# Kernel optimization log

Measured on AMD Instinct MI355X. Metric: run time of the kernel, lower is better.

## Reference

```python
import jax, jax.numpy as jnp
import numpy as np

SEQ, B, IN, H, L = 2048, 64, 512, 512, 2

def _xavier(key, shape):
    fan_out, fan_in = shape
    bound = float(np.sqrt(6.0 / (fan_in + fan_out)))
    return jax.random.uniform(key, shape, jnp.float32, -bound, bound)

def setup_inputs() -> dict:
    key = jax.random.key(0)
    ks = jax.random.split(key, 5)
    x = jax.random.normal(ks[0], (SEQ, B, IN), jnp.float32)
    # layer 0: input_size=IN; layer 1: input_size=H. Biases init to zeros (reset_parameters).
    return {
        "x": x,
        "W_ih0": _xavier(ks[1], (H, IN)),
        "W_hh0": _xavier(ks[2], (H, H)),
        "b_ih0": jnp.zeros((H,), jnp.float32),
        "b_hh0": jnp.zeros((H,), jnp.float32),
        "W_ih1": _xavier(ks[3], (H, H)),
        "W_hh1": _xavier(ks[4], (H, H)),
        "b_ih1": jnp.zeros((H,), jnp.float32),
        "b_hh1": jnp.zeros((H,), jnp.float32),
    }

def _run_layer(x_in, W_ih, W_hh, b_ih, b_hh):
    # Precompute input projection for all timesteps (matches forward_optimized / same math as forward).
    proj = jnp.einsum('sbi,hi->sbh', x_in, W_ih) + b_ih  # [S,B,H]
    h0 = jnp.zeros((x_in.shape[1], W_hh.shape[0]), x_in.dtype)
    def step(h, p_t):
        h_new = jnp.tanh(p_t + h @ W_hh.T + b_hh)
        return h_new, h_new
    h_final, outs = jax.lax.scan(step, h0, proj)
    return outs, h_final

def reference(x, W_ih0, W_hh0, b_ih0, b_hh0, W_ih1, W_hh1, b_ih1, b_hh1):
    out0, h0 = _run_layer(x, W_ih0, W_hh0, b_ih0, b_hh0)
    out1, h1 = _run_layer(out0, W_ih1, W_hh1, b_ih1, b_hh1)
    hidden = jnp.stack([h0, h1], axis=0)  # [num_layers, B, H]
    return out1, hidden
```

## Files before the change

kernel.cpp:

```cpp
#include <hip/hip_runtime.h>
#include <cstdint>
#include <cstddef>

#define SEQ   2048
#define BATCH 64
#define HID   512

__global__ __launch_bounds__(256)
void proj_gemm(const float* __restrict__ A, const float* __restrict__ W,
               const float* __restrict__ bias, float* __restrict__ C)
{
    __shared__ float As[16][132];
    __shared__ float Bs[16][132];
    const int t  = threadIdx.x;
    const int bm = blockIdx.x >> 2;
    const int bn = blockIdx.x & 3;
    const int m0 = bm * 128;
    const int n0 = bn * 128;
    const int tn = t & 15;
    const int tm = t >> 4;

    float acc[8][8];
#pragma unroll
    for (int i = 0; i < 8; ++i)
#pragma unroll
        for (int j = 0; j < 8; ++j) acc[i][j] = 0.f;

    const int lrow = t >> 2;
    const int lk4  = t & 3;

    for (int kk = 0; kk < 512; kk += 16) {
#pragma unroll
        for (int i = 0; i < 2; ++i) {
            const int row = lrow + i * 64;
            float4 va = *(const float4*)&A[(size_t)(m0 + row) * 512 + kk + lk4 * 4];
            As[lk4 * 4 + 0][row] = va.x;
            As[lk4 * 4 + 1][row] = va.y;
            As[lk4 * 4 + 2][row] = va.z;
            As[lk4 * 4 + 3][row] = va.w;
            float4 vb = *(const float4*)&W[(size_t)(n0 + row) * 512 + kk + lk4 * 4];
            Bs[lk4 * 4 + 0][row] = vb.x;
            Bs[lk4 * 4 + 1][row] = vb.y;
            Bs[lk4 * 4 + 2][row] = vb.z;
            Bs[lk4 * 4 + 3][row] = vb.w;
        }
        __syncthreads();
#pragma unroll
        for (int k = 0; k < 16; ++k) {
            float4 a0 = *(const float4*)&As[k][tm * 8];
            float4 a1 = *(const float4*)&As[k][tm * 8 + 4];
            float4 b0 = *(const float4*)&Bs[k][tn * 4];
            float4 b1 = *(const float4*)&Bs[k][64 + tn * 4];
            float ar[8] = {a0.x, a0.y, a0.z, a0.w, a1.x, a1.y, a1.z, a1.w};
            float bc[8] = {b0.x, b0.y, b0.z, b0.w, b1.x, b1.y, b1.z, b1.w};
#pragma unroll
            for (int i = 0; i < 8; ++i)
#pragma unroll
                for (int j = 0; j < 8; ++j)
                    acc[i][j] = fmaf(ar[i], bc[j], acc[i][j]);
        }
        __syncthreads();
    }

    float4 bv0 = *(const float4*)&bias[n0 + tn * 4];
    float4 bv1 = *(const float4*)&bias[n0 + 64 + tn * 4];
    const float bb[8] = {bv0.x, bv0.y, bv0.z, bv0.w, bv1.x, bv1.y, bv1.z, bv1.w};
#pragma unroll
    for (int i = 0; i < 8; ++i) {
        const size_t rowoff = (size_t)(m0 + tm * 8 + i) * 512 + n0;
        float4 o0, o1;
        o0.x = acc[i][0] + bb[0]; o0.y = acc[i][1] + bb[1];
        o0.z = acc[i][2] + bb[2]; o0.w = acc[i][3] + bb[3];
        o1.x = acc[i][4] + bb[4]; o1.y = acc[i][5] + bb[5];
        o1.z = acc[i][6] + bb[6]; o1.w = acc[i][7] + bb[7];
        *(float4*)&C[rowoff + tn * 4] = o0;
        *(float4*)&C[rowoff + 64 + tn * 4] = o1;
    }
}

__device__ __forceinline__ float fast_tanh(float x)
{
    const float e = __builtin_amdgcn_exp2f(x * 2.88539008177793f);
    return fmaf(-2.0f, __builtin_amdgcn_rcpf(e + 1.0f), 1.0f);
}

#define WLD(i)  const float4 w##i = wb[(i) * 64]
#define WFMA(i, accA, accB) do { \
    const float4 hp = h0[i]; const float4 hq = h1[i]; \
    accA = fmaf(w##i.x, hp.x, accA); accA = fmaf(w##i.y, hp.y, accA); \
    accA = fmaf(w##i.z, hp.z, accA); accA = fmaf(w##i.w, hp.w, accA); \
    accB = fmaf(w##i.x, hq.x, accB); accB = fmaf(w##i.y, hq.y, accB); \
    accB = fmaf(w##i.z, hq.z, accB); accB = fmaf(w##i.w, hq.w, accB); } while (0)

__global__ __launch_bounds__(512, 2)
void rnn_scan(const float* __restrict__ proj, const float* __restrict__ Whh,
              const float* __restrict__ bhh, float* __restrict__ out,
              float* __restrict__ hidden, unsigned long long* __restrict__ hbuf)
{
    extern __shared__ float lds[];
    float4* Wv4 = (float4*)lds;
    float4* hS4 = (float4*)(lds + 32768);
    float*  hSf = lds + 32768;

    const int t    = threadIdx.x;
    const int bid  = blockIdx.x;
    const int g    = bid & 31;
    const int s    = bid >> 5;
    const int b0   = g * 2;
    const int base = s * 64;
    const int w    = t >> 6;
    const int l    = t & 63;
    const int rr   = l & 7;
    const int kc   = l >> 3;
    const int row  = base + w * 8 + rr;

    const float4* Wg4 = (const float4*)Whh;
    {
        const int k0 = kc * 16;
#pragma unroll
        for (int j = 0; j < 16; ++j)
            Wv4[w * 1024 + j * 64 + l] = Wg4[(size_t)row * 128 + k0 + j];
    }
    const bool pub  = (kc < 2);
    const float breg = pub ? bhh[row] : 0.f;

    for (int i = t; i < 2176; i += 512) hSf[i] = 0.f;
    __syncthreads();

    const bool own  = (t >= base) && (t < base + 64);
    const int  pado = (t >> 6) * 68 + (t & 63);

    float pv_next = 0.f;
    if (pub) pv_next = proj[(size_t)(b0 + kc) * HID + row];

    unsigned long long* gb = hbuf + (size_t)g * 4096;
    const float4* wb = Wv4 + w * 1024 + l;

    for (int step = 0; step < SEQ; ++step) {
        const int p = step & 1;

        const float pv = pv_next;
        if (pub && step + 1 < SEQ)
            pv_next = proj[((size_t)(step + 1) * BATCH + (b0 + kc)) * HID + row];

        WLD(0);  WLD(1);  WLD(2);  WLD(3);
        WLD(4);  WLD(5);  WLD(6);  WLD(7);
        WLD(8);  WLD(9);  WLD(10); WLD(11);
        WLD(12); WLD(13); WLD(14); WLD(15);
        __builtin_amdgcn_sched_barrier(0);

        if (!own) {
            const unsigned int want = (unsigned int)step;
            const unsigned long long* f0 = gb + (size_t)p * 2048 + t;
            const unsigned long long* f1 = f0 + 512;
            unsigned long long x0 = 0, x1 = 0;
            bool ok0 = false, ok1 = false;
            int spins = 0;
            for (;;) {
                if (!ok0) {
                    x0 = __hip_atomic_load(f0, __ATOMIC_RELAXED, __HIP_MEMORY_SCOPE_AGENT);
                    ok0 = (unsigned int)(x0 >> 32) == want;
                }
                if (!ok1) {
                    x1 = __hip_atomic_load(f1, __ATOMIC_RELAXED, __HIP_MEMORY_SCOPE_AGENT);
                    ok1 = (unsigned int)(x1 >> 32) == want;
                }
                if (ok0 & ok1) break;
                __builtin_amdgcn_s_sleep(1);
                if (++spins > 4096) {
                    __builtin_amdgcn_fence(__ATOMIC_ACQUIRE, "agent");
                    spins = 0;
                }
            }
            hSf[p * 1088 + pado]       = __uint_as_float((unsigned int)x0);
            hSf[p * 1088 + 544 + pado] = __uint_as_float((unsigned int)x1);
        }
        __syncthreads();

        const float4* h0 = hS4 + p * 272 + kc * 17;
        const float4* h1 = h0 + 136;
        float a0e = 0.f, a0o = 0.f, a1e = 0.f, a1o = 0.f;
        WFMA(0,  a0e, a1e); WFMA(1,  a0o, a1o);
        WFMA(2,  a0e, a1e); WFMA(3,  a0o, a1o);
        WFMA(4,  a0e, a1e); WFMA(5,  a0o, a1o);
        WFMA(6,  a0e, a1e); WFMA(7,  a0o, a1o);
        WFMA(8,  a0e, a1e); WFMA(9,  a0o, a1o);
        WFMA(10, a0e, a1e); WFMA(11, a0o, a1o);
        WFMA(12, a0e, a1e); WFMA(13, a0o, a1o);
        WFMA(14, a0e, a1e); WFMA(15, a0o, a1o);
        float s0 = a0e + a0o;
        float s1 = a1e + a1o;
        s0 += __shfl_xor(s0, 8, 64);  s1 += __shfl_xor(s1, 8, 64);
        s0 += __shfl_xor(s0, 16, 64); s1 += __shfl_xor(s1, 16, 64);
        s0 += __shfl_xor(s0, 32, 64); s1 += __shfl_xor(s1, 32, 64);

        if (pub) {
            const float sum = (kc == 0) ? s0 : s1;
            const int   bb  = b0 + kc;
            const float hn  = fast_tanh(pv + breg + sum);
            out[((size_t)step * BATCH + bb) * HID + row] = hn;
            const unsigned long long pk =
                ((unsigned long long)(unsigned int)(step + 1) << 32) |
                (unsigned long long)__float_as_uint(hn);
            __hip_atomic_store(gb + (size_t)(p ^ 1) * 2048 + (size_t)kc * 512 + row,
                               pk, __ATOMIC_RELAXED, __HIP_MEMORY_SCOPE_AGENT);
            hSf[(p ^ 1) * 1088 + kc * 544 + (row >> 6) * 68 + (row & 63)] = hn;
            if (step == SEQ - 1) hidden[(size_t)bb * HID + row] = hn;
        }
    }
}

extern "C" void kernel_launch(void* const* d_in, const int* in_sizes, int n_in,
                              void* d_out, int out_size, void* d_ws, size_t ws_size,
                              hipStream_t stream)
{
    (void)in_sizes; (void)n_in; (void)out_size; (void)ws_size;

    const float* x    = (const float*)d_in[0];
    const float* Wih0 = (const float*)d_in[1];
    const float* Whh0 = (const float*)d_in[2];
    const float* bih0 = (const float*)d_in[3];
    const float* bhh0 = (const float*)d_in[4];
    const float* Wih1 = (const float*)d_in[5];
    const float* Whh1 = (const float*)d_in[6];
    const float* bih1 = (const float*)d_in[7];
    const float* bhh1 = (const float*)d_in[8];

    float* out1   = (float*)d_out;
    float* hidden = out1 + (size_t)SEQ * BATCH * HID;

    float* proj = (float*)d_ws;
    unsigned long long* hbufA = (unsigned long long*)(proj + (size_t)SEQ * BATCH * HID);
    unsigned long long* hbufB = hbufA + (size_t)32 * 4096;

    hipMemsetAsync(hbufA, 0, (size_t)2 * 32 * 4096 * sizeof(unsigned long long),
                   stream);

    const size_t shmem = (size_t)(32768 + 2176) * sizeof(float);
    (void)hipFuncSetAttribute((const void*)rnn_scan,
                              hipFuncAttributeMaxDynamicSharedMemorySize, (int)shmem);

    proj_gemm<<<dim3(4096), dim3(256), 0, stream>>>(x, Wih0, bih0, proj);
    {
        const float* p = proj; const float* w = Whh0; const float* bb = bhh0;
        float* o = out1; float* hd = hidden; unsigned long long* hb = hbufA;
        void* args[] = {&p, &w, &bb, &o, &hd, &hb};
        hipLaunchCooperativeKernel((const void*)rnn_scan, dim3(256), dim3(512),
                                   args, (unsigned)shmem, stream);
    }

    proj_gemm<<<dim3(4096), dim3(256), 0, stream>>>(out1, Wih1, bih1, proj);
    {
        const float* p = proj; const float* w = Whh1; const float* bb = bhh1;
        float* o = out1; float* hd = hidden + BATCH * HID; unsigned long long* hb = hbufB;
        void* args[] = {&p, &w, &bb, &o, &hd, &hb};
        hipLaunchCooperativeKernel((const void*)rnn_scan, dim3(256), dim3(512),
                                   args, (unsigned)shmem, stream);
    }
}
```

Measured before the change: 9.570 ms.

## Stream bf16-converted recurrent weights from global memory instead of LDS

W_hh is pre-converted into a permuted bf16 layout by a new conversion kernel. Each scan step now reads those weights straight from global memory with inline-asm dwordx2 loads, instead of staging the fp32 weights in 128KB of LDS. The goal is to halve the weight bytes per step and free LDS, issuing the loads early so they overlap the cross-block spin-wait. In exchange, weight reads now go to L2 on the sequential critical path every step. bf16 rounding of the recurrent weights accumulates error over 2048 steps. The inline-asm loads also rely on implicit waitcnts being inserted before their results are used.

Result: slower. 13.55 ms (+41.6%).

```diff
diff --git a/kernel.cpp b/kernel.cpp
--- a/kernel.cpp
+++ b/kernel.cpp
@@ -78,29 +78,51 @@
     }
 }
 
+__device__ __forceinline__ unsigned short f2bf(float f)
+{
+    const unsigned int u = __float_as_uint(f);
+    return (unsigned short)((u + 0x7fffu + ((u >> 16) & 1u)) >> 16);
+}
+
+__global__ __launch_bounds__(256)
+void conv_bf16(const float* __restrict__ W, ushort4* __restrict__ dst)
+{
+    const int i   = blockIdx.x * 256 + threadIdx.x;
+    const int row = i & 511;
+    const int kj  = i >> 9;
+    const int k0  = ((kj >> 4) << 6) | ((kj & 15) << 2);
+    const float4 v = *(const float4*)&W[(size_t)row * 512 + k0];
+    ushort4 o;
+    o.x = f2bf(v.x); o.y = f2bf(v.y); o.z = f2bf(v.z); o.w = f2bf(v.w);
+    dst[i] = o;
+}
+
 __device__ __forceinline__ float fast_tanh(float x)
 {
     const float e = __builtin_amdgcn_exp2f(x * 2.88539008177793f);
     return fmaf(-2.0f, __builtin_amdgcn_rcpf(e + 1.0f), 1.0f);
 }
 
-#define WLD(i)  const float4 w##i = wb[(i) * 64]
+#define WISSUE(i) asm volatile("global_load_dwordx2 %0, %1, off" \
+                               : "=v"(wv##i) : "v"(wb + (i) * 512))
 #define WFMA(i, accA, accB) do { \
-    const float4 hp = h0[i]; const float4 hq = h1[i]; \
-    accA = fmaf(w##i.x, hp.x, accA); accA = fmaf(w##i.y, hp.y, accA); \
-    accA = fmaf(w##i.z, hp.z, accA); accA = fmaf(w##i.w, hp.w, accA); \
-    accB = fmaf(w##i.x, hq.x, accB); accB = fmaf(w##i.y, hq.y, accB); \
-    accB = fmaf(w##i.z, hq.z, accB); accB = fmaf(w##i.w, hq.w, accB); } while (0)
+    const float4 ha = h0[i]; const float4 hb = h1[i]; \
+    const float f0 = __uint_as_float(wv##i.x << 16); \
+    const float f1 = __uint_as_float(wv##i.x & 0xffff0000u); \
+    const float f2 = __uint_as_float(wv##i.y << 16); \
+    const float f3 = __uint_as_float(wv##i.y & 0xffff0000u); \
+    accA = fmaf(f0, ha.x, accA); accA = fmaf(f1, ha.y, accA); \
+    accA = fmaf(f2, ha.z, accA); accA = fmaf(f3, ha.w, accA); \
+    accB = fmaf(f0, hb.x, accB); accB = fmaf(f1, hb.y, accB); \
+    accB = fmaf(f2, hb.z, accB); accB = fmaf(f3, hb.w, accB); } while (0)
 
 __global__ __launch_bounds__(512, 2)
-void rnn_scan(const float* __restrict__ proj, const float* __restrict__ Whh,
+void rnn_scan(const float* __restrict__ proj, const ushort4* __restrict__ Wbf,
               const float* __restrict__ bhh, float* __restrict__ out,
               float* __restrict__ hidden, unsigned long long* __restrict__ hbuf)
 {
-    extern __shared__ float lds[];
-    float4* Wv4 = (float4*)lds;
-    float4* hS4 = (float4*)(lds + 32768);
-    float*  hSf = lds + 32768;
+    __shared__ float hSf[2176];
+    float4* hS4 = (float4*)hSf;
 
     const int t    = threadIdx.x;
     const int bid  = blockIdx.x;
@@ -111,17 +133,10 @@
     const int w    = t >> 6;
     const int l    = t & 63;
     const int rr   = l & 7;
-    const int kc   = l >> 3;
+    const int kq   = l >> 3;
     const int row  = base + w * 8 + rr;
 
-    const float4* Wg4 = (const float4*)Whh;
-    {
-        const int k0 = kc * 16;
-#pragma unroll
-        for (int j = 0; j < 16; ++j)
-            Wv4[w * 1024 + j * 64 + l] = Wg4[(size_t)row * 128 + k0 + j];
-    }
-    const bool pub  = (kc < 2);
+    const bool pub  = (kq < 2);
     const float breg = pub ? bhh[row] : 0.f;
 
     for (int i = t; i < 2176; i += 512) hSf[i] = 0.f;
@@ -131,23 +146,24 @@
     const int  pado = (t >> 6) * 68 + (t & 63);
 
     float pv_next = 0.f;
-    if (pub) pv_next = proj[(size_t)(b0 + kc) * HID + row];
+    if (pub) pv_next = proj[(size_t)(b0 + kq) * HID + row];
 
     unsigned long long* gb = hbuf + (size_t)g * 4096;
-    const float4* wb = Wv4 + w * 1024 + l;
+    const ushort4* wb = Wbf + (size_t)(kq << 4) * 512 + row;
 
     for (int step = 0; step < SEQ; ++step) {
         const int p = step & 1;
 
         const float pv = pv_next;
         if (pub && step + 1 < SEQ)
-            pv_next = proj[((size_t)(step + 1) * BATCH + (b0 + kc)) * HID + row];
-
-        WLD(0);  WLD(1);  WLD(2);  WLD(3);
-        WLD(4);  WLD(5);  WLD(6);  WLD(7);
-        WLD(8);  WLD(9);  WLD(10); WLD(11);
-        WLD(12); WLD(13); WLD(14); WLD(15);
-        __builtin_amdgcn_sched_barrier(0);
+            pv_next = proj[((size_t)(step + 1) * BATCH + (b0 + kq)) * HID + row];
+
+        uint2 wv0, wv1, wv2, wv3, wv4, wv5, wv6, wv7;
+        uint2 wv8, wv9, wv10, wv11, wv12, wv13, wv14, wv15;
+        WISSUE(0);  WISSUE(1);  WISSUE(2);  WISSUE(3);
+        WISSUE(4);  WISSUE(5);  WISSUE(6);  WISSUE(7);
+        WISSUE(8);  WISSUE(9);  WISSUE(10); WISSUE(11);
+        WISSUE(12); WISSUE(13); WISSUE(14); WISSUE(15);
 
         if (!own) {
             const unsigned int want = (unsigned int)step;
@@ -177,7 +193,7 @@
         }
         __syncthreads();
 
-        const float4* h0 = hS4 + p * 272 + kc * 17;
+        const float4* h0 = hS4 + p * 272 + kq * 17;
         const float4* h1 = h0 + 136;
         float a0e = 0.f, a0o = 0.f, a1e = 0.f, a1o = 0.f;
         WFMA(0,  a0e, a1e); WFMA(1,  a0o, a1o);
@@ -195,16 +211,16 @@
         s0 += __shfl_xor(s0, 32, 64); s1 += __shfl_xor(s1, 32, 64);
 
         if (pub) {
-            const float sum = (kc == 0) ? s0 : s1;
-            const int   bb  = b0 + kc;
+            const float sum = (kq == 0) ? s0 : s1;
+            const int   bb  = b0 + kq;
             const float hn  = fast_tanh(pv + breg + sum);
             out[((size_t)step * BATCH + bb) * HID + row] = hn;
             const unsigned long long pk =
                 ((unsigned long long)(unsigned int)(step + 1) << 32) |
                 (unsigned long long)__float_as_uint(hn);
-            __hip_atomic_store(gb + (size_t)(p ^ 1) * 2048 + (size_t)kc * 512 + row,
+            __hip_atomic_store(gb + (size_t)(p ^ 1) * 2048 + (size_t)kq * 512 + row,
                                pk, __ATOMIC_RELAXED, __HIP_MEMORY_SCOPE_AGENT);
-            hSf[(p ^ 1) * 1088 + kc * 544 + (row >> 6) * 68 + (row & 63)] = hn;
+            hSf[(p ^ 1) * 1088 + kq * 544 + (row >> 6) * 68 + (row & 63)] = hn;
             if (step == SEQ - 1) hidden[(size_t)bb * HID + row] = hn;
         }
     }
@@ -232,29 +248,30 @@
     float* proj = (float*)d_ws;
     unsigned long long* hbufA = (unsigned long long*)(proj + (size_t)SEQ * BATCH * HID);
     unsigned long long* hbufB = hbufA + (size_t)32 * 4096;
+    ushort4* Wbf0 = (ushort4*)(hbufB + (size_t)32 * 4096);
+    ushort4* Wbf1 = Wbf0 + 65536;
 
     hipMemsetAsync(hbufA, 0, (size_t)2 * 32 * 4096 * sizeof(unsigned long long),
                    stream);
 
-    const size_t shmem = (size_t)(32768 + 2176) * sizeof(float);
-    (void)hipFuncSetAttribute((const void*)rnn_scan,
-                              hipFuncAttributeMaxDynamicSharedMemorySize, (int)shmem);
+    conv_bf16<<<dim3(256), dim3(256), 0, stream>>>(Whh0, Wbf0);
+    conv_bf16<<<dim3(256), dim3(256), 0, stream>>>(Whh1, Wbf1);
 
     proj_gemm<<<dim3(4096), dim3(256), 0, stream>>>(x, Wih0, bih0, proj);
     {
-        const float* p = proj; const float* w = Whh0; const float* bb = bhh0;
+        const float* p = proj; const ushort4* wv = Wbf0; const float* bb = bhh0;
         float* o = out1; float* hd = hidden; unsigned long long* hb = hbufA;
-        void* args[] = {&p, &w, &bb, &o, &hd, &hb};
+        void* args[] = {&p, &wv, &bb, &o, &hd, &hb};
         hipLaunchCooperativeKernel((const void*)rnn_scan, dim3(256), dim3(512),
-                                   args, (unsigned)shmem, stream);
+                                   args, 0, stream);
     }
 
     proj_gemm<<<dim3(4096), dim3(256), 0, stream>>>(out1, Wih1, bih1, proj);
     {
-        const float* p = proj; const float* w = Whh1; const float* bb = bhh1;
+        const float* p = proj; const ushort4* wv = Wbf1; const float* bb = bhh1;
         float* o = out1; float* hd = hidden + BATCH * HID; unsigned long long* hb = hbufB;
-        void* args[] = {&p, &w, &bb, &o, &hd, &hb};
+        void* args[] = {&p, &wv, &bb, &o, &hd, &hb};
         hipLaunchCooperativeKernel((const void*)rnn_scan, dim3(256), dim3(512),
-                                   args, (unsigned)shmem, stream);
-    }
-}
+                                   args, 0, stream);
+    }
+}
```
